# Performance work log

Measured on AMD Instinct MI355X. Metric: run time of the kernel, lower is better.

## Reference

```python
import jax, jax.numpy as jnp
import numpy as np

HEADS = 16
EMBED = 1024
HEAD_DIM = EMBED // HEADS


def setup_inputs() -> dict:
    key = jax.random.key(0)
    ks = jax.random.split(key, 7)
    B, S, E = 2, 2048, EMBED
    scale = 1.0 / np.sqrt(E)
    return {
        "query": jax.random.normal(ks[0], (B, S, E), dtype=jnp.float32),
        "key": jax.random.normal(ks[1], (B, S, E), dtype=jnp.float32),
        "value": jax.random.normal(ks[2], (B, S, E), dtype=jnp.float32),
        # nn.Linear(E, E, bias=False) weights, applied as x @ W.T
        "Wq": jax.random.normal(ks[3], (E, E), dtype=jnp.float32) * scale,
        "Wk": jax.random.normal(ks[4], (E, E), dtype=jnp.float32) * scale,
        "Wv": jax.random.normal(ks[5], (E, E), dtype=jnp.float32) * scale,
        "Wo": jax.random.normal(ks[6], (E, E), dtype=jnp.float32) * scale,
    }


def reference(query, key, value, Wq, Wk, Wv, Wo):
    B, S, E = query.shape
    H, D = HEADS, HEAD_DIM

    def split_heads(x, W):
        # [B,S,E] @ W.T -> [B,S,E] -> [B,H,S,D]
        return (x @ W.T).reshape(B, -1, H, D).transpose(0, 2, 1, 3)

    q = split_heads(query, Wq)
    k = split_heads(key, Wk)
    v = split_heads(value, Wv)

    scores = jnp.einsum("bhqd,bhkd->bhqk", q, k) / jnp.sqrt(jnp.float32(D))
    attn = jax.nn.softmax(scores, axis=-1)  # [B,H,S,S]
    x = jnp.einsum("bhqk,bhkd->bhqd", attn, v)
    x = x.transpose(0, 2, 1, 3).reshape(B, -1, H * D)
    return x @ Wo.T
```

## Files before the change

### kernel.cpp

```cpp
#include <hip/hip_runtime.h>
#include <hip/hip_bf16.h>


typedef __attribute__((ext_vector_type(8))) short short8;
typedef __attribute__((ext_vector_type(4))) float f32x4;
typedef __attribute__((ext_vector_type(4))) unsigned short us4;
typedef __attribute__((ext_vector_type(4))) int i32x4;

#define MFMA16(a, b, c) __builtin_amdgcn_mfma_f32_16x16x32_bf16(a, b, c, 0, 0, 0)

static constexpr int B = 2;
static constexpr int S = 2048;
static constexpr int E = 1024;
static constexpr int H = 16;
static constexpr int D = 64;
static constexpr int M = B * S;
static constexpr size_t NE = (size_t)M * E;
static constexpr size_t NW = (size_t)E * E;

static __device__ __forceinline__ unsigned short f2bf(float x) {
  unsigned int u = __float_as_uint(x);
  unsigned int r = (u + 0x7FFFu + ((u >> 16) & 1u)) >> 16;
  return (unsigned short)r;
}

static __device__ __forceinline__ int cvt_pk_bf16(float lo, float hi) {
  int r;
  asm("v_cvt_pk_bf16_f32 %0, %1, %2" : "=v"(r) : "v"(lo), "v"(hi));
  return r;
}

static __device__ __forceinline__ void gload_lds16(const unsigned short* g,
                                                   unsigned short* l) {
  __builtin_amdgcn_global_load_lds(
      (const __attribute__((address_space(1))) unsigned int*)g,
      (__attribute__((address_space(3))) unsigned int*)l, 16, 0, 0);
}

__global__ void cvt_all_kernel(const float* __restrict__ s0,
                               const float* __restrict__ s1,
                               const float* __restrict__ s2,
                               const float* __restrict__ s3,
                               const float* __restrict__ s4,
                               const float* __restrict__ s5,
                               const float* __restrict__ s6,
                               unsigned short* __restrict__ d0,
                               unsigned short* __restrict__ d1,
                               unsigned short* __restrict__ d2,
                               unsigned short* __restrict__ d3,
                               unsigned short* __restrict__ d4,
                               unsigned short* __restrict__ d5,
                               unsigned short* __restrict__ d6, int nAct4,
                               int nW4) {
  const int z = blockIdx.y;
  const float* srcs[7] = {s0, s1, s2, s3, s4, s5, s6};
  unsigned short* dsts[7] = {d0, d1, d2, d3, d4, d5, d6};
  const float* src = srcs[z];
  unsigned short* dst = dsts[z];
  const int n4 = (z < 3) ? nAct4 : nW4;
  for (int i = blockIdx.x * blockDim.x + threadIdx.x; i < n4;
       i += gridDim.x * blockDim.x) {
    float4 v = reinterpret_cast<const float4*>(src)[i];
    ushort4 o;
    o.x = f2bf(v.x); o.y = f2bf(v.y); o.z = f2bf(v.z); o.w = f2bf(v.w);
    reinterpret_cast<ushort4*>(dst)[i] = o;
  }
}

__global__ __launch_bounds__(256) void gemm_proj_kernel(
    const unsigned short* __restrict__ xq, const unsigned short* __restrict__ xk,
    const unsigned short* __restrict__ xv, const unsigned short* __restrict__ wq,
    const unsigned short* __restrict__ wk, const unsigned short* __restrict__ wv,
    unsigned short* __restrict__ Qh, unsigned short* __restrict__ Kh,
    unsigned short* __restrict__ Vt) {
  __shared__ __align__(16) unsigned short As[2][128 * 32];
  __shared__ __align__(16) unsigned short Bs[2][128 * 32];

  const int which = blockIdx.z;
  const unsigned short* A = (which == 0) ? xq : ((which == 1) ? xk : xv);
  const unsigned short* W = (which == 0) ? wq : ((which == 1) ? wk : wv);

  const int wave = threadIdx.x >> 6;
  const int lane = threadIdx.x & 63;
  const int lr = lane & 15;
  const int lk = (lane >> 4) * 8;
  const int m0 = blockIdx.x * 128;
  const int n0 = blockIdx.y * 128;
  const int wm = (wave >> 1) * 64;
  const int wn = (wave & 1) * 64;
  const int srow = lane >> 2;
  const int scol = (lane & 3) * 8;

  f32x4 acc[4][4];
  const f32x4 fz = {0.f, 0.f, 0.f, 0.f};
#pragma unroll
  for (int i = 0; i < 4; ++i)
#pragma unroll
    for (int j = 0; j < 4; ++j) acc[i][j] = fz;

#define STAGE_G(bb, kk)                                                       \
  {                                                                           \
    _Pragma("unroll") for (int i = 0; i < 2; ++i) {                           \
      const int c = wave * 2 + i;                                             \
      const int row = c * 16 + srow;                                          \
      gload_lds16(A + (size_t)(m0 + row) * E + (kk) + scol, &As[bb][c * 512]);\
      gload_lds16(W + (size_t)(n0 + row) * E + (kk) + scol, &Bs[bb][c * 512]);\
    }                                                                         \
  }

  STAGE_G(0, 0);
  __syncthreads();
  int buf = 0;
  for (int kk = 0; kk < E; kk += 32) {
    if (kk + 32 < E) STAGE_G(buf ^ 1, kk + 32);
    short8 af[4], bw[4];
#pragma unroll
    for (int i = 0; i < 4; ++i)
      af[i] = *reinterpret_cast<const short8*>(
          &As[buf][(wm + i * 16 + lr) * 32 + lk]);
#pragma unroll
    for (int j = 0; j < 4; ++j)
      bw[j] = *reinterpret_cast<const short8*>(
          &Bs[buf][(wn + j * 16 + lr) * 32 + lk]);
#pragma unroll
    for (int i = 0; i < 4; ++i)
#pragma unroll
      for (int j = 0; j < 4; ++j) acc[i][j] = MFMA16(af[i], bw[j], acc[i][j]);
    __syncthreads();
    buf ^= 1;
  }
#undef STAGE_G

  const int rbase = (lane >> 4) * 4;
#pragma unroll
  for (int i = 0; i < 4; ++i) {
#pragma unroll
    for (int j = 0; j < 4; ++j) {
      const int col = n0 + wn + j * 16 + lr;
      const int h = col >> 6, d = col & 63;
#pragma unroll
      for (int r = 0; r < 4; ++r) {
        const int row = m0 + wm + i * 16 + rbase + r;
        const int b = row >> 11, s = row & (S - 1);
        const float v = acc[i][j][r];
        if (which == 0) {
          Qh[(((size_t)b * H + h) * S + s) * D + d] = f2bf(v * 0.18033688f);
        } else if (which == 1) {
          Kh[(((size_t)b * H + h) * S + s) * D + d] = f2bf(v);
        } else {
          Vt[(((size_t)b * H + h) * D + d) * S + s] = f2bf(v);
        }
      }
    }
  }
}

__global__ __launch_bounds__(256) void gemm_out_kernel(
    const unsigned short* __restrict__ X, const unsigned short* __restrict__ Wo,
    float* __restrict__ out) {
  __shared__ __align__(16) unsigned short As[2][128 * 32];
  __shared__ __align__(16) unsigned short Bs[2][64 * 32];

  const int wave = threadIdx.x >> 6;
  const int lane = threadIdx.x & 63;
  const int lr = lane & 15;
  const int lk = (lane >> 4) * 8;
  const int m0 = blockIdx.x * 128;
  const int n0 = blockIdx.y * 64;
  const int wm = (wave >> 1) * 64;
  const int wn = (wave & 1) * 32;
  const int srow = lane >> 2;
  const int scol = (lane & 3) * 8;

  f32x4 acc[4][2];
  const f32x4 fz = {0.f, 0.f, 0.f, 0.f};
#pragma unroll
  for (int i = 0; i < 4; ++i)
#pragma unroll
    for (int j = 0; j < 2; ++j) acc[i][j] = fz;

#define STAGE_O(bb, kk)                                                       \
  {                                                                           \
    _Pragma("unroll") for (int i = 0; i < 2; ++i) {                           \
      const int c = wave * 2 + i;                                             \
      const int row = c * 16 + srow;                                          \
      gload_lds16(X + (size_t)(m0 + row) * E + (kk) + scol, &As[bb][c * 512]);\
    }                                                                         \
    gload_lds16(Wo + (size_t)(n0 + wave * 16 + srow) * E + (kk) + scol,       \
                &Bs[bb][wave * 512]);                                         \
  }

  STAGE_O(0, 0);
  __syncthreads();
  int buf = 0;
  for (int kk = 0; kk < E; kk += 32) {
    if (kk + 32 < E) STAGE_O(buf ^ 1, kk + 32);
    short8 af[4], bw[2];
#pragma unroll
    for (int i = 0; i < 4; ++i)
      af[i] = *reinterpret_cast<const short8*>(
          &As[buf][(wm + i * 16 + lr) * 32 + lk]);
#pragma unroll
    for (int j = 0; j < 2; ++j)
      bw[j] = *reinterpret_cast<const short8*>(
          &Bs[buf][(wn + j * 16 + lr) * 32 + lk]);
#pragma unroll
    for (int i = 0; i < 4; ++i)
#pragma unroll
      for (int j = 0; j < 2; ++j) acc[i][j] = MFMA16(af[i], bw[j], acc[i][j]);
    __syncthreads();
    buf ^= 1;
  }
#undef STAGE_O

  const int rbase = (lane >> 4) * 4;
#pragma unroll
  for (int i = 0; i < 4; ++i) {
#pragma unroll
    for (int j = 0; j < 2; ++j) {
      const int col = n0 + wn + j * 16 + lr;
#pragma unroll
      for (int r = 0; r < 4; ++r) {
        const int row = m0 + wm + i * 16 + rbase + r;
        out[(size_t)row * E + col] = acc[i][j][r];
      }
    }
  }
}

__global__ __launch_bounds__(128) void attn_kernel(
    const unsigned short* __restrict__ Qh, const unsigned short* __restrict__ Kh,
    const unsigned short* __restrict__ Vt, unsigned short* __restrict__ Xb) {
  __shared__ __align__(16) unsigned short Ks[2][64 * 64];
  __shared__ __align__(16) unsigned short Vs[2][64 * 64];

  const int wave = threadIdx.x >> 6;
  const int lane = threadIdx.x & 63;
  const int lr = lane & 15;
  const int jj = lane >> 4;
  const int lk = jj * 8;

  const int lin = blockIdx.x + (blockIdx.y << 4);
  const int nlin = (lin & 7) * 64 + (lin >> 3);
  const int qt = nlin & 15;
  const int bh = nlin >> 4;
  const int q0 = qt * 128 + wave * 64;

  short8 qf[4][2];
#pragma unroll
  for (int g = 0; g < 4; ++g) {
    const unsigned short* Qp = Qh + ((size_t)bh * S + q0 + g * 16) * D;
    qf[g][0] = *reinterpret_cast<const short8*>(Qp + (size_t)lr * D + lk);
    qf[g][1] = *reinterpret_cast<const short8*>(Qp + (size_t)lr * D + 32 + lk);
  }

  const unsigned short* Kbase = Kh + (size_t)bh * S * D;
  const unsigned short* Vbase = Vt + (size_t)bh * D * S;

  const f32x4 fz = {0.f, 0.f, 0.f, 0.f};
  float mrun[4], lsum[4];
  f32x4 acc[4][4];
#pragma unroll
  for (int g = 0; g < 4; ++g) {
    mrun[g] = -3.0e38f;
    lsum[g] = 0.f;
#pragma unroll
    for (int dt = 0; dt < 4; ++dt) acc[g][dt] = fz;
  }

  const int srow = lane >> 3;
  const int sgV = (lane & 7) ^ srow;

#define STAGE_KV(bb, kt)                                                      \
  {                                                                           \
    _Pragma("unroll") for (int i = 0; i < 4; ++i) {                           \
      const int c = wave * 4 + i;                                             \
      const int sgK = (lane & 7) ^ ((srow & 3) | ((c & 1) << 2));             \
      gload_lds16(Kbase + (size_t)((kt) + c * 8 + srow) * D + sgK * 8,        \
                  &Ks[bb][c * 512]);                                          \
      gload_lds16(Vbase + (size_t)(c * 8 + srow) * S + (kt) + sgV * 8,        \
                  &Vs[bb][c * 512]);                                          \
    }                                                                         \
  }

  STAGE_KV(0, 0);
  __syncthreads();
  int buf = 0;

  const int rb = ((lr >> 2) << 3) + (lr & 3);
  const int kswz = (lr & 3) | (((lr >> 2) & 1) << 2);
  const int vswz = lr & 7;

  constexpr int NT = S / 64;
  for (int t = 0; t < NT; ++t) {
    if (t + 1 < NT) STAGE_KV(buf ^ 1, (t + 1) * 64);

    short8 kf0[4], kf1[4], vf0[4], vf1[4];
#pragma unroll
    for (int nt = 0; nt < 4; ++nt) {
      const int r = rb + ((nt & 1) << 2) + ((nt >> 1) << 5);
      kf0[nt] = *reinterpret_cast<const short8*>(
          &Ks[buf][r * 64 + ((jj ^ kswz) * 8)]);
      kf1[nt] = *reinterpret_cast<const short8*>(
          &Ks[buf][r * 64 + (((jj + 4) ^ kswz) * 8)]);
    }
#pragma unroll
    for (int dt = 0; dt < 4; ++dt) {
      const int r = dt * 16 + lr;
      vf0[dt] = *reinterpret_cast<const short8*>(
          &Vs[buf][r * 64 + ((jj ^ vswz) * 8)]);
      vf1[dt] = *reinterpret_cast<const short8*>(
          &Vs[buf][r * 64 + (((jj + 4) ^ vswz) * 8)]);
    }

#pragma unroll
    for (int g = 0; g < 4; ++g) {
      f32x4 sf[4];
      __builtin_amdgcn_s_setprio(1);
#pragma unroll
      for (int nt = 0; nt < 4; ++nt) {
        f32x4 z = fz;
        z = MFMA16(kf0[nt], qf[g][0], z);
        z = MFMA16(kf1[nt], qf[g][1], z);
        sf[nt] = z;
      }
      __builtin_amdgcn_s_setprio(0);

      float mx = sf[0][0];
#pragma unroll
      for (int nt = 0; nt < 4; ++nt)
#pragma unroll
        for (int r = 0; r < 4; ++r) mx = fmaxf(mx, sf[nt][r]);
      mx = fmaxf(mx, __shfl_xor(mx, 16));
      mx = fmaxf(mx, __shfl_xor(mx, 32));

      if (__any(mx > mrun[g] + 8.f)) {
        const float nm = fmaxf(mrun[g], mx);
        const float fac = __builtin_amdgcn_exp2f(mrun[g] - nm);
        mrun[g] = nm;
        lsum[g] *= fac;
#pragma unroll
        for (int dt = 0; dt < 4; ++dt)
#pragma unroll
          for (int r = 0; r < 4; ++r) acc[g][dt][r] *= fac;
      }

#pragma unroll
      for (int nt = 0; nt < 4; ++nt)
#pragma unroll
        for (int r = 0; r < 4; ++r) {
          sf[nt][r] = __builtin_amdgcn_exp2f(sf[nt][r] - mrun[g]);
          lsum[g] += sf[nt][r];
        }
      i32x4 w0, w1;
      w0.x = cvt_pk_bf16(sf[0][0], sf[0][1]);
      w0.y = cvt_pk_bf16(sf[0][2], sf[0][3]);
      w0.z = cvt_pk_bf16(sf[1][0], sf[1][1]);
      w0.w = cvt_pk_bf16(sf[1][2], sf[1][3]);
      w1.x = cvt_pk_bf16(sf[2][0], sf[2][1]);
      w1.y = cvt_pk_bf16(sf[2][2], sf[2][3]);
      w1.z = cvt_pk_bf16(sf[3][0], sf[3][1]);
      w1.w = cvt_pk_bf16(sf[3][2], sf[3][3]);
      const short8 pa0 = __builtin_bit_cast(short8, w0);
      const short8 pa1 = __builtin_bit_cast(short8, w1);

      __builtin_amdgcn_s_setprio(1);
#pragma unroll
      for (int dt = 0; dt < 4; ++dt) {
        acc[g][dt] = MFMA16(vf0[dt], pa0, acc[g][dt]);
        acc[g][dt] = MFMA16(vf1[dt], pa1, acc[g][dt]);
      }
      __builtin_amdgcn_s_setprio(0);
    }

    __syncthreads();
    buf ^= 1;
  }
#undef STAGE_KV

  const int b = bh >> 4, h = bh & (H - 1);
#pragma unroll
  for (int g = 0; g < 4; ++g) {
    float ltot = lsum[g];
    ltot += __shfl_xor(ltot, 16);
    ltot += __shfl_xor(ltot, 32);
    const float inv = 1.0f / ltot;
    const int row = q0 + g * 16 + lr;
#pragma unroll
    for (int dt = 0; dt < 4; ++dt) {
      us4 o;
#pragma unroll
      for (int r = 0; r < 4; ++r) o[r] = f2bf(acc[g][dt][r] * inv);
      *reinterpret_cast<us4*>(
          &Xb[((size_t)b * S + row) * E + h * D + dt * 16 + 4 * jj]) = o;
    }
  }
}

extern "C" void kernel_launch(void* const* d_in, const int* in_sizes, int n_in,
                              void* d_out, int out_size, void* d_ws, size_t ws_size,
                              hipStream_t stream) {
  const float* q_f = (const float*)d_in[0];
  const float* k_f = (const float*)d_in[1];
  const float* v_f = (const float*)d_in[2];
  const float* wq_f = (const float*)d_in[3];
  const float* wk_f = (const float*)d_in[4];
  const float* wv_f = (const float*)d_in[5];
  const float* wo_f = (const float*)d_in[6];

  unsigned short* xq = (unsigned short*)d_ws;
  unsigned short* xk = xq + NE;
  unsigned short* xv = xk + NE;
  unsigned short* wq = xv + NE;
  unsigned short* wk = wq + NW;
  unsigned short* wv = wk + NW;
  unsigned short* wo = wv + NW;
  unsigned short* Qh = wo + NW;
  unsigned short* Kh = Qh + NE;
  unsigned short* Vt = Kh + NE;
  unsigned short* Xb = Vt + NE;

  cvt_all_kernel<<<dim3(512, 7), 256, 0, stream>>>(
      q_f, k_f, v_f, wq_f, wk_f, wv_f, wo_f, xq, xk, xv, wq, wk, wv, wo,
      (int)(NE / 4), (int)(NW / 4));

  gemm_proj_kernel<<<dim3(M / 128, E / 128, 3), 256, 0, stream>>>(
      xq, xk, xv, wq, wk, wv, Qh, Kh, Vt);

  attn_kernel<<<dim3(S / 128, B * H), 128, 0, stream>>>(Qh, Kh, Vt, Xb);

  gemm_out_kernel<<<dim3(M / 128, E / 64), 256, 0, stream>>>(Xb, wo,
                                                             (float*)d_out);
}
```

Measured before the change: 163.3 us.

## Split attention KV range across two wave pairs and merge partial softmax states

The attention block now uses 4 waves: two pairs each process half of the key/value sequence for the same 128 queries, and their partial outputs, maxima and sums are merged through shared memory at the end (split-K flash attention within a block). The row sum is computed with an extra MFMA against a ones vector instead of scalar adds, and all QK^T scores for a tile are computed up front per K fragment. Global pointers are precomputed and incremented. This aims to raise occupancy and latency hiding on the attention kernel, at the cost of doubled LDS, more registers for sf[4][4], and an extra merge pass with a barrier.

Measured after the change: 161.2 us. No clear change (-1.3%).

```diff
diff --git a/kernel.cpp b/kernel.cpp
--- a/kernel.cpp
+++ b/kernel.cpp
@@ -228,23 +228,25 @@
   }
 }
 
-__global__ __launch_bounds__(128) void attn_kernel(
+__global__ __launch_bounds__(256) void attn_kernel(
     const unsigned short* __restrict__ Qh, const unsigned short* __restrict__ Kh,
     const unsigned short* __restrict__ Vt, unsigned short* __restrict__ Xb) {
-  __shared__ __align__(16) unsigned short Ks[2][64 * 64];
-  __shared__ __align__(16) unsigned short Vs[2][64 * 64];
+  __shared__ __align__(16) unsigned short SM[2][2][2][64 * 64];
 
   const int wave = threadIdx.x >> 6;
   const int lane = threadIdx.x & 63;
   const int lr = lane & 15;
   const int jj = lane >> 4;
   const int lk = jj * 8;
+  const int qg = wave & 1;
+  const int half = wave >> 1;
+  constexpr int S2 = S / 2;
 
   const int lin = blockIdx.x + (blockIdx.y << 4);
   const int nlin = (lin & 7) * 64 + (lin >> 3);
   const int qt = nlin & 15;
   const int bh = nlin >> 4;
-  const int q0 = qt * 128 + wave * 64;
+  const int q0 = qt * 128 + qg * 64;
 
   short8 qf[4][2];
 #pragma unroll
@@ -258,12 +260,15 @@
   const unsigned short* Vbase = Vt + (size_t)bh * D * S;
 
   const f32x4 fz = {0.f, 0.f, 0.f, 0.f};
-  float mrun[4], lsum[4];
-  f32x4 acc[4][4];
+  const short8 ones = {(short)0x3F80, (short)0x3F80, (short)0x3F80,
+                       (short)0x3F80, (short)0x3F80, (short)0x3F80,
+                       (short)0x3F80, (short)0x3F80};
+  float mrun[4];
+  f32x4 acc[4][4], lacc[4];
 #pragma unroll
   for (int g = 0; g < 4; ++g) {
     mrun[g] = -3.0e38f;
-    lsum[g] = 0.f;
+    lacc[g] = fz;
 #pragma unroll
     for (int dt = 0; dt < 4; ++dt) acc[g][dt] = fz;
   }
@@ -271,19 +276,28 @@
   const int srow = lane >> 3;
   const int sgV = (lane & 7) ^ srow;
 
-#define STAGE_KV(bb, kt)                                                      \
+  const unsigned short* kptr[4];
+  const unsigned short* vptr[4];
+#pragma unroll
+  for (int i = 0; i < 4; ++i) {
+    const int c = qg * 4 + i;
+    const int sgK = (lane & 7) ^ ((srow & 3) | ((c & 1) << 2));
+    kptr[i] = Kbase + (size_t)(half * S2 + c * 8 + srow) * D + sgK * 8;
+    vptr[i] = Vbase + (size_t)(c * 8 + srow) * S + half * S2 + sgV * 8;
+  }
+
+#define STAGE_KV(bb)                                                          \
   {                                                                           \
     _Pragma("unroll") for (int i = 0; i < 4; ++i) {                           \
-      const int c = wave * 4 + i;                                             \
-      const int sgK = (lane & 7) ^ ((srow & 3) | ((c & 1) << 2));             \
-      gload_lds16(Kbase + (size_t)((kt) + c * 8 + srow) * D + sgK * 8,        \
-                  &Ks[bb][c * 512]);                                          \
-      gload_lds16(Vbase + (size_t)(c * 8 + srow) * S + (kt) + sgV * 8,        \
-                  &Vs[bb][c * 512]);                                          \
+      const int c = qg * 4 + i;                                               \
+      gload_lds16(kptr[i], &SM[0][half][bb][c * 512]);                        \
+      gload_lds16(vptr[i], &SM[1][half][bb][c * 512]);                        \
+      kptr[i] += 64 * D;                                                      \
+      vptr[i] += 64;                                                          \
     }                                                                         \
   }
 
-  STAGE_KV(0, 0);
+  STAGE_KV(0);
   __syncthreads();
   int buf = 0;
 
@@ -291,76 +305,73 @@
   const int kswz = (lr & 3) | (((lr >> 2) & 1) << 2);
   const int vswz = lr & 7;
 
-  constexpr int NT = S / 64;
-  for (int t = 0; t < NT; ++t) {
-    if (t + 1 < NT) STAGE_KV(buf ^ 1, (t + 1) * 64);
-
-    short8 kf0[4], kf1[4], vf0[4], vf1[4];
+  constexpr int NT2 = S2 / 64;
+  for (int t = 0; t < NT2; ++t) {
+    if (t + 1 < NT2) STAGE_KV(buf ^ 1);
+
+    f32x4 sf[4][4];
+    __builtin_amdgcn_s_setprio(1);
 #pragma unroll
     for (int nt = 0; nt < 4; ++nt) {
       const int r = rb + ((nt & 1) << 2) + ((nt >> 1) << 5);
-      kf0[nt] = *reinterpret_cast<const short8*>(
-          &Ks[buf][r * 64 + ((jj ^ kswz) * 8)]);
-      kf1[nt] = *reinterpret_cast<const short8*>(
-          &Ks[buf][r * 64 + (((jj + 4) ^ kswz) * 8)]);
-    }
+      short8 kf0 = *reinterpret_cast<const short8*>(
+          &SM[0][half][buf][r * 64 + ((jj ^ kswz) * 8)]);
+      short8 kf1 = *reinterpret_cast<const short8*>(
+          &SM[0][half][buf][r * 64 + (((jj + 4) ^ kswz) * 8)]);
+#pragma unroll
+      for (int g = 0; g < 4; ++g) {
+        f32x4 z = fz;
+        z = MFMA16(kf0, qf[g][0], z);
+        z = MFMA16(kf1, qf[g][1], z);
+        sf[g][nt] = z;
+      }
+    }
+    __builtin_amdgcn_s_setprio(0);
+
+    short8 vf0[4], vf1[4];
 #pragma unroll
     for (int dt = 0; dt < 4; ++dt) {
       const int r = dt * 16 + lr;
       vf0[dt] = *reinterpret_cast<const short8*>(
-          &Vs[buf][r * 64 + ((jj ^ vswz) * 8)]);
+          &SM[1][half][buf][r * 64 + ((jj ^ vswz) * 8)]);
       vf1[dt] = *reinterpret_cast<const short8*>(
-          &Vs[buf][r * 64 + (((jj + 4) ^ vswz) * 8)]);
+          &SM[1][half][buf][r * 64 + (((jj + 4) ^ vswz) * 8)]);
     }
 
 #pragma unroll
     for (int g = 0; g < 4; ++g) {
-      f32x4 sf[4];
-      __builtin_amdgcn_s_setprio(1);
-#pragma unroll
-      for (int nt = 0; nt < 4; ++nt) {
-        f32x4 z = fz;
-        z = MFMA16(kf0[nt], qf[g][0], z);
-        z = MFMA16(kf1[nt], qf[g][1], z);
-        sf[nt] = z;
-      }
-      __builtin_amdgcn_s_setprio(0);
-
-      float mx = sf[0][0];
+      float tm[4];
 #pragma unroll
       for (int nt = 0; nt < 4; ++nt)
-#pragma unroll
-        for (int r = 0; r < 4; ++r) mx = fmaxf(mx, sf[nt][r]);
+        tm[nt] = fmaxf(fmaxf(sf[g][nt][0], sf[g][nt][1]),
+                       fmaxf(sf[g][nt][2], sf[g][nt][3]));
+      float mx = fmaxf(fmaxf(tm[0], tm[1]), fmaxf(tm[2], tm[3]));
       mx = fmaxf(mx, __shfl_xor(mx, 16));
       mx = fmaxf(mx, __shfl_xor(mx, 32));
-
       if (__any(mx > mrun[g] + 8.f)) {
         const float nm = fmaxf(mrun[g], mx);
         const float fac = __builtin_amdgcn_exp2f(mrun[g] - nm);
         mrun[g] = nm;
-        lsum[g] *= fac;
+        lacc[g] *= fac;
 #pragma unroll
         for (int dt = 0; dt < 4; ++dt)
 #pragma unroll
           for (int r = 0; r < 4; ++r) acc[g][dt][r] *= fac;
       }
-
 #pragma unroll
       for (int nt = 0; nt < 4; ++nt)
 #pragma unroll
-        for (int r = 0; r < 4; ++r) {
-          sf[nt][r] = __builtin_amdgcn_exp2f(sf[nt][r] - mrun[g]);
-          lsum[g] += sf[nt][r];
-        }
+        for (int r = 0; r < 4; ++r)
+          sf[g][nt][r] = __builtin_amdgcn_exp2f(sf[g][nt][r] - mrun[g]);
       i32x4 w0, w1;
-      w0.x = cvt_pk_bf16(sf[0][0], sf[0][1]);
-      w0.y = cvt_pk_bf16(sf[0][2], sf[0][3]);
-      w0.z = cvt_pk_bf16(sf[1][0], sf[1][1]);
-      w0.w = cvt_pk_bf16(sf[1][2], sf[1][3]);
-      w1.x = cvt_pk_bf16(sf[2][0], sf[2][1]);
-      w1.y = cvt_pk_bf16(sf[2][2], sf[2][3]);
-      w1.z = cvt_pk_bf16(sf[3][0], sf[3][1]);
-      w1.w = cvt_pk_bf16(sf[3][2], sf[3][3]);
+      w0.x = cvt_pk_bf16(sf[g][0][0], sf[g][0][1]);
+      w0.y = cvt_pk_bf16(sf[g][0][2], sf[g][0][3]);
+      w0.z = cvt_pk_bf16(sf[g][1][0], sf[g][1][1]);
+      w0.w = cvt_pk_bf16(sf[g][1][2], sf[g][1][3]);
+      w1.x = cvt_pk_bf16(sf[g][2][0], sf[g][2][1]);
+      w1.y = cvt_pk_bf16(sf[g][2][2], sf[g][2][3]);
+      w1.z = cvt_pk_bf16(sf[g][3][0], sf[g][3][1]);
+      w1.w = cvt_pk_bf16(sf[g][3][2], sf[g][3][3]);
       const short8 pa0 = __builtin_bit_cast(short8, w0);
       const short8 pa1 = __builtin_bit_cast(short8, w1);
 
@@ -370,6 +381,8 @@
         acc[g][dt] = MFMA16(vf0[dt], pa0, acc[g][dt]);
         acc[g][dt] = MFMA16(vf1[dt], pa1, acc[g][dt]);
       }
+      lacc[g] = MFMA16(ones, pa0, lacc[g]);
+      lacc[g] = MFMA16(ones, pa1, lacc[g]);
       __builtin_amdgcn_s_setprio(0);
     }
 
@@ -378,21 +391,41 @@
   }
 #undef STAGE_KV
 
-  const int b = bh >> 4, h = bh & (H - 1);
-#pragma unroll
-  for (int g = 0; g < 4; ++g) {
-    float ltot = lsum[g];
-    ltot += __shfl_xor(ltot, 16);
-    ltot += __shfl_xor(ltot, 32);
-    const float inv = 1.0f / ltot;
-    const int row = q0 + g * 16 + lr;
-#pragma unroll
-    for (int dt = 0; dt < 4; ++dt) {
-      us4 o;
-#pragma unroll
-      for (int r = 0; r < 4; ++r) o[r] = f2bf(acc[g][dt][r] * inv);
-      *reinterpret_cast<us4*>(
-          &Xb[((size_t)b * S + row) * E + h * D + dt * 16 + 4 * jj]) = o;
+  float* Mg = (float*)&SM[0][0][0][0];
+  if (half == 1) {
+    float* p = Mg + (size_t)(qg * 64 + lane) * 73;
+#pragma unroll
+    for (int g = 0; g < 4; ++g) {
+#pragma unroll
+      for (int dt = 0; dt < 4; ++dt)
+#pragma unroll
+        for (int r = 0; r < 4; ++r) p[g * 16 + dt * 4 + r] = acc[g][dt][r];
+      p[64 + g] = mrun[g];
+      p[68 + g] = lacc[g][0];
+    }
+  }
+  __syncthreads();
+  if (half == 0) {
+    const float* p = Mg + (size_t)(qg * 64 + lane) * 73;
+    const int b = bh >> 4, h = bh & (H - 1);
+#pragma unroll
+    for (int g = 0; g < 4; ++g) {
+      const float mB = p[64 + g];
+      const float lB = p[68 + g];
+      const float nm = fmaxf(mrun[g], mB);
+      const float fa = __builtin_amdgcn_exp2f(mrun[g] - nm);
+      const float fb = __builtin_amdgcn_exp2f(mB - nm);
+      const float inv = 1.0f / (lacc[g][0] * fa + lB * fb);
+      const int row = q0 + g * 16 + lr;
+#pragma unroll
+      for (int dt = 0; dt < 4; ++dt) {
+        us4 o;
+#pragma unroll
+        for (int r = 0; r < 4; ++r)
+          o[r] = f2bf((acc[g][dt][r] * fa + p[g * 16 + dt * 4 + r] * fb) * inv);
+        *reinterpret_cast<us4*>(
+            &Xb[((size_t)b * S + row) * E + h * D + dt * 16 + 4 * jj]) = o;
+      }
     }
   }
 }
@@ -427,7 +460,7 @@
   gemm_proj_kernel<<<dim3(M / 128, E / 128, 3), 256, 0, stream>>>(
       xq, xk, xv, wq, wk, wv, Qh, Kh, Vt);
 
-  attn_kernel<<<dim3(S / 128, B * H), 128, 0, stream>>>(Qh, Kh, Vt, Xb);
+  attn_kernel<<<dim3(S / 128, B * H), 256, 0, stream>>>(Qh, Kh, Vt, Xb);
 
   gemm_out_kernel<<<dim3(M / 128, E / 64), 256, 0, stream>>>(Xb, wo,
                                                              (float*)d_out);
```
